# Optimization experiments

Measured on AMD Instinct MI355X. Metric: run time of the kernel, lower is better.

Reference implementation:

```python
import jax, jax.numpy as jnp
import numpy as np

N, T, H, O, S, R = 64, 1024, 256, 80, 128, 2


def _lin(k, fin, fout):
    kw, kb = jax.random.split(k)
    s = 1.0 / np.sqrt(fin)
    return (jax.random.uniform(kw, (fout, fin), jnp.float32, -s, s),
            jax.random.uniform(kb, (fout,), jnp.float32, -s, s))


def _gru_params(k, fin, hid):
    k1, k2, k3, k4 = jax.random.split(k, 4)
    s = 1.0 / np.sqrt(hid)
    u = lambda kk, shp: jax.random.uniform(kk, shp, jnp.float32, -s, s)
    return u(k1, (3 * hid, fin)), u(k2, (3 * hid, hid)), u(k3, (3 * hid,)), u(k4, (3 * hid,))


def setup_inputs() -> dict:
    key = jax.random.key(0)
    ks = jax.random.split(key, 16)
    inp = {}
    inp["input_enc"] = jax.random.normal(ks[0], (N, T, 2 * H), jnp.float32)
    inp["input_attW_enc"] = jax.random.normal(ks[1], (N, T, 2 * H), jnp.float32)
    inp["input_dec"] = jax.random.normal(ks[2], (N, O), jnp.float32)
    inp["style_vec"] = jax.random.normal(ks[3], (N, 1, S), jnp.float32)
    lengths = jnp.sort(jax.random.randint(ks[4], (N,), 1, T + 1))[::-1]
    inp["lengths_enc"] = lengths.at[0].set(T)  # pack_padded requires max(len)==T, descending
    inp["pw1"], inp["pb1"] = _lin(ks[5], O, 2 * H)
    inp["pw2"], inp["pb2"] = _lin(ks[6], 2 * H, H)
    inp["wdec"], inp["bdec"] = _lin(ks[7], 2 * H, 2 * H)
    inp["ga_ih"], inp["ga_hh"], inp["ga_bih"], inp["ga_bhh"] = _gru_params(ks[8], 3 * H + S, 2 * H)
    inp["wattn"], inp["battn"] = _lin(ks[9], 2 * H, 1)
    inp["wsc"], inp["bsc"] = _lin(ks[10], 4 * H + S, 2 * H)
    inp["g1_ih"], inp["g1_hh"], inp["g1_bih"], inp["g1_bhh"] = _gru_params(ks[11], 4 * H + S, 2 * H)
    inp["g2_ih"], inp["g2_hh"], inp["g2_bih"], inp["g2_bhh"] = _gru_params(ks[12], 2 * H, 2 * H)
    inp["wout"], inp["bout"] = _lin(ks[13], 2 * H, R * O)
    return inp


def _gru_cell(x, h, w_ih, w_hh, b_ih, b_hh):
    # PyTorch GRU cell: gates order (r, z, n)
    gi = x @ w_ih.T + b_ih
    gh = h @ w_hh.T + b_hh
    ir, iz, inn = jnp.split(gi, 3, -1)
    hr, hz, hn = jnp.split(gh, 3, -1)
    r = jax.nn.sigmoid(ir + hr)
    z = jax.nn.sigmoid(iz + hz)
    n = jnp.tanh(inn + r * hn)
    return (1.0 - z) * n + z * h


def reference(input_enc, input_attW_enc, input_dec, style_vec,
              pw1, pb1, pw2, pb2, wdec, bdec,
              ga_ih, ga_hh, ga_bih, ga_bhh,
              wattn, battn, wsc, bsc,
              g1_ih, g1_hh, g1_bih, g1_bhh,
              g2_ih, g2_hh, g2_bih, g2_bhh,
              wout, bout, lengths_enc):
    Nn, Tt, D2 = input_enc.shape
    Hh = D2 // 2
    # prenet (dropout disabled: eval-mode reference)
    pre = jax.nn.relu(jax.nn.relu(input_dec @ pw1.T + pb1) @ pw2.T + pb2)  # (N,H)
    ctx0 = jnp.zeros((Nn, 2 * Hh), input_enc.dtype)  # input_context=None -> zeros
    sv = style_vec[:, 0, :]
    x_att = jnp.concatenate([pre, ctx0, sv], axis=-1)  # (N,3H+S)
    h0 = jnp.zeros((Nn, 2 * Hh), input_enc.dtype)  # hidden states start None -> zeros
    out_att = _gru_cell(x_att, h0, ga_ih, ga_hh, ga_bih, ga_bhh)  # (N,2H)
    attW_dec = out_att @ wdec.T + bdec  # (N,2H), broadcast over T (expand_as)
    e = jnp.tanh(input_attW_enc + attW_dec[:, None, :])  # (N,T,2H)
    score = e @ wattn.T + battn  # (N,T,1)
    mask = (jnp.arange(Tt)[None, :] < lengths_enc[:, None]).astype(score.dtype)[..., None]
    w = jnp.exp(score) * mask  # pack/pad zeroes padded positions
    w = w / jnp.maximum(jnp.sum(w, axis=1, keepdims=True), 1e-12)  # F.normalize(p=1, dim=1)
    attn_applied = jnp.einsum('nt,ntd->nd', w[..., 0], input_enc)  # bmm(w^T, enc) -> (N,2H)
    out_dec = jnp.concatenate([attn_applied, out_att, sv], axis=-1)  # (N,4H+S)
    residual = out_dec @ wsc.T + bsc
    h1 = _gru_cell(out_dec, h0, g1_ih, g1_hh, g1_bih, g1_bhh)
    residual = residual + h1
    h2 = _gru_cell(residual, h0, g2_ih, g2_hh, g2_bih, g2_bhh)
    residual = residual + h2
    output = (residual @ wout.T + bout).reshape(Nn, R, -1)  # (N,r,O)
    return output, attn_applied[:, None, :]
```

## Files before the change

### kernel.cpp

```cpp
#include <hip/hip_runtime.h>
#include <math.h>

#define NB  64
#define TT  1024
#define H2  512
#define SS  128
#define OO  80
#define FIN_A 896
#define FIN_1 1152
#define CH  32

__device__ __forceinline__ float fast_rcp(float x) { return __builtin_amdgcn_rcpf(x); }
__device__ __forceinline__ float fast_sigmoid(float x) { return fast_rcp(1.0f + __expf(-x)); }
__device__ __forceinline__ float fast_tanh(float x) {
    float e = __expf(2.0f * x);
    return 1.0f - 2.0f * fast_rcp(e + 1.0f);
}
__device__ __forceinline__ float wred(float p) {
    #pragma unroll
    for (int o = 32; o > 0; o >>= 1) p += __shfl_xor(p, o, 64);
    return p;
}

__global__ void k_l1(const float* __restrict__ xdec, const float* __restrict__ pw1,
                     const float* __restrict__ pb1, const float* __restrict__ sv,
                     float* __restrict__ t1T, float* __restrict__ xaT,
                     float* __restrict__ out_decT) {
    int wv = threadIdx.x >> 6, lane = threadIdx.x & 63;
    if (blockIdx.x < 128) {
        int i = blockIdx.x * 4 + wv;
        const float* w = pw1 + i * OO;
        const float* x = xdec + lane * OO;
        float acc = 0.0f;
        #pragma unroll 8
        for (int k = 0; k < OO; ++k) acc += w[k] * x[k];
        t1T[i * 64 + lane] = fmaxf(acc + pb1[i], 0.0f);
    } else {
        int s = (blockIdx.x - 128) * 4 + wv;
        float v = sv[lane * SS + s];
        xaT[(256 + s) * 64 + lane] = v;
        out_decT[(1024 + s) * 64 + lane] = v;
    }
}

__global__ __launch_bounds__(512) void k_l2(const float* __restrict__ t1T,
                                            const float* __restrict__ pw2,
                                            const float* __restrict__ pb2,
                                            float* __restrict__ xaT) {
    int i = blockIdx.x;
    int wv = threadIdx.x >> 6, lane = threadIdx.x & 63;
    int k0 = wv * 64;
    const float* w = pw2 + (size_t)i * H2 + k0;
    const float* xT = t1T + k0 * 64;
    float p = 0.0f;
    #pragma unroll 8
    for (int k = 0; k < 64; ++k) p += w[k] * xT[k * 64 + lane];
    __shared__ float s[8][64];
    s[wv][lane] = p;
    __syncthreads();
    if (wv == 0) {
        float acc = 0.0f;
        #pragma unroll
        for (int q = 0; q < 8; ++q) acc += s[q][lane];
        xaT[i * 64 + lane] = fmaxf(acc + pb2[i], 0.0f);
    }
}

__global__ __launch_bounds__(512) void k_gruA(const float* __restrict__ xaT,
                                              const float* __restrict__ ga_ih,
                                              const float* __restrict__ ga_bih,
                                              const float* __restrict__ ga_bhh,
                                              float* __restrict__ out_decT) {
    int j = blockIdx.x;
    int wv = threadIdx.x >> 6, lane = threadIdx.x & 63;
    int k0 = wv * 48;
    const float* wr = ga_ih + (size_t)j * FIN_A;
    const float* wz = ga_ih + (size_t)(H2 + j) * FIN_A;
    const float* wn = ga_ih + (size_t)(2 * H2 + j) * FIN_A;
    float pr = 0.0f, pz = 0.0f, pn = 0.0f;
    #pragma unroll 8
    for (int kk = 0; kk < 48; ++kk) {
        int k = k0 + kk;
        int wc = k + (k >= 256 ? 512 : 0);
        float xv = xaT[k * 64 + lane];
        pr += wr[wc] * xv; pz += wz[wc] * xv; pn += wn[wc] * xv;
    }
    __shared__ float s[3][8][64];
    s[0][wv][lane] = pr; s[1][wv][lane] = pz; s[2][wv][lane] = pn;
    __syncthreads();
    if (wv == 0) {
        float fr = 0.0f, fz = 0.0f, fn = 0.0f;
        #pragma unroll
        for (int q = 0; q < 8; ++q) { fr += s[0][q][lane]; fz += s[1][q][lane]; fn += s[2][q][lane]; }
        float r = fast_sigmoid(fr + ga_bih[j] + ga_bhh[j]);
        float z = fast_sigmoid(fz + ga_bih[H2 + j] + ga_bhh[H2 + j]);
        float nn = fast_tanh(fn + ga_bih[2 * H2 + j] + r * ga_bhh[2 * H2 + j]);
        out_decT[(H2 + j) * 64 + lane] = (1.0f - z) * nn;
    }
}

__global__ __launch_bounds__(512) void k_attw(const float* __restrict__ out_decT,
                                              const float* __restrict__ wdec,
                                              const float* __restrict__ bdec,
                                              float* __restrict__ attW_dec) {
    int i = blockIdx.x;
    int wv = threadIdx.x >> 6, lane = threadIdx.x & 63;
    int k0 = wv * 64;
    const float* w = wdec + (size_t)i * H2 + k0;
    const float* xT = out_decT + (H2 + k0) * 64;
    float p = 0.0f;
    #pragma unroll 8
    for (int k = 0; k < 64; ++k) p += w[k] * xT[k * 64 + lane];
    __shared__ float s[8][64];
    s[wv][lane] = p;
    __syncthreads();
    if (wv == 0) {
        float acc = 0.0f;
        #pragma unroll
        for (int q = 0; q < 8; ++q) acc += s[q][lane];
        attW_dec[lane * H2 + i] = acc + bdec[i];
    }
}

__global__ __launch_bounds__(256, 8) void k_attn(
        const float* __restrict__ enc, const float* __restrict__ attw_enc,
        const float* __restrict__ attW_dec, const float* __restrict__ wattn,
        const float* __restrict__ battn, const int* __restrict__ lengths,
        float* __restrict__ num_part ,
        float* __restrict__ den_part ) {
    int n = blockIdx.y, c = blockIdx.x;
    int wv = threadIdx.x >> 6, lane = threadIdx.x & 63;
    int t0 = c * (TT / CH);
    int len = lengths[n];
    __shared__ float sew[TT / CH];
    __shared__ float s[4 * 512];
    __shared__ float sd[4];

    {
        const float4* d4 = (const float4*)(attW_dec + n * H2);
        const float4* w4 = (const float4*)wattn;
        float b = battn[0];
        #pragma unroll
        for (int r = 0; r < 8; ++r) {
            int t = t0 + wv * 8 + r;
            float val = 0.0f;
            if (t < len) {
                const float4* e4 = (const float4*)(attw_enc + ((size_t)(n * TT + t)) * H2);
                float p = 0.0f;
                #pragma unroll
                for (int m = 0; m < 2; ++m) {
                    int idx = lane + m * 64;
                    float4 e = e4[idx], d = d4[idx], w = w4[idx];
                    p += fast_tanh(e.x + d.x) * w.x + fast_tanh(e.y + d.y) * w.y +
                         fast_tanh(e.z + d.z) * w.z + fast_tanh(e.w + d.w) * w.w;
                }
                p = wred(p);
                val = __expf(p + b);
            }
            if (lane == 0) sew[wv * 8 + r] = val;
        }
    }
    __syncthreads();

    int d0 = lane * 8;
    const float* base = enc + ((size_t)(n * TT + t0 + wv * 8)) * H2 + d0;
    float4 a0 = {0, 0, 0, 0}, a1 = {0, 0, 0, 0};
    float dp = 0.0f;
    #pragma unroll
    for (int r = 0; r < 8; ++r) {
        float wt = sew[wv * 8 + r];
        if (wt != 0.0f) {
            const float4* v4 = (const float4*)(base + (size_t)r * H2);
            float4 v0 = v4[0], v1 = v4[1];
            a0.x += wt * v0.x; a0.y += wt * v0.y; a0.z += wt * v0.z; a0.w += wt * v0.w;
            a1.x += wt * v1.x; a1.y += wt * v1.y; a1.z += wt * v1.z; a1.w += wt * v1.w;
            dp += wt;
        }
    }
    float4* srow = (float4*)(s + wv * 512 + d0);
    srow[0] = a0; srow[1] = a1;
    if (lane == 0) sd[wv] = dp;
    __syncthreads();
    int d = threadIdx.x;
    float r0 = s[d] + s[512 + d] + s[1024 + d] + s[1536 + d];
    float r1 = s[256 + d] + s[768 + d] + s[1280 + d] + s[1792 + d];
    num_part[((size_t)c * H2 + d) * 64 + n] = r0;
    num_part[((size_t)c * H2 + 256 + d) * 64 + n] = r1;
    if (threadIdx.x == 0) den_part[c * NB + n] = sd[0] + sd[1] + sd[2] + sd[3];
}

__global__ void k_reduce(const float* __restrict__ num_part, const float* __restrict__ den_part,
                         float* __restrict__ out, float* __restrict__ out_decT) {
    int d = blockIdx.x * 4 + (threadIdx.x >> 6);
    int lane = threadIdx.x & 63;
    float s = 0.0f, den = 0.0f;
    #pragma unroll 8
    for (int c = 0; c < CH; ++c) {
        s += num_part[((size_t)c * H2 + d) * 64 + lane];
        den += den_part[c * NB + lane];
    }
    float a = s / fmaxf(den, 1e-12f);
    out_decT[d * 64 + lane] = a;
    out[NB * 160 + lane * H2 + d] = a;
}

__global__ __launch_bounds__(512) void k_sc_h1(const float* __restrict__ out_decT,
                                               const float* __restrict__ wsc,
                                               const float* __restrict__ bsc,
                                               const float* __restrict__ g1_ih,
                                               const float* __restrict__ g1_bih,
                                               const float* __restrict__ g1_bhh,
                                               float* __restrict__ res1T) {
    int j = blockIdx.x;
    int wv = threadIdx.x >> 6, lane = threadIdx.x & 63;
    int k0 = wv * 144;
    const float* ws_ = wsc + (size_t)j * FIN_1 + k0;
    const float* wr = g1_ih + (size_t)j * FIN_1 + k0;
    const float* wz = g1_ih + (size_t)(H2 + j) * FIN_1 + k0;
    const float* wn = g1_ih + (size_t)(2 * H2 + j) * FIN_1 + k0;
    const float* xT = out_decT + k0 * 64;
    float2 ps = {0, 0}, pr = {0, 0}, pz = {0, 0}, pn = {0, 0};
    #pragma unroll 4
    for (int k = 0; k < 144; k += 2) {
        float x0 = xT[k * 64 + lane];
        float x1 = xT[(k + 1) * 64 + lane];
        float2 a = *(const float2*)(ws_ + k);
        float2 b = *(const float2*)(wr + k);
        float2 cc = *(const float2*)(wz + k);
        float2 dd = *(const float2*)(wn + k);
        ps.x += a.x * x0; ps.y += a.y * x1;
        pr.x += b.x * x0; pr.y += b.y * x1;
        pz.x += cc.x * x0; pz.y += cc.y * x1;
        pn.x += dd.x * x0; pn.y += dd.y * x1;
    }
    __shared__ float s[4][8][64];
    s[0][wv][lane] = ps.x + ps.y; s[1][wv][lane] = pr.x + pr.y;
    s[2][wv][lane] = pz.x + pz.y; s[3][wv][lane] = pn.x + pn.y;
    __syncthreads();
    if (wv == 0) {
        float fs = 0.0f, fr = 0.0f, fz = 0.0f, fn = 0.0f;
        #pragma unroll
        for (int q = 0; q < 8; ++q) {
            fs += s[0][q][lane]; fr += s[1][q][lane];
            fz += s[2][q][lane]; fn += s[3][q][lane];
        }
        float r = fast_sigmoid(fr + g1_bih[j] + g1_bhh[j]);
        float z = fast_sigmoid(fz + g1_bih[H2 + j] + g1_bhh[H2 + j]);
        float nn = fast_tanh(fn + g1_bih[2 * H2 + j] + r * g1_bhh[2 * H2 + j]);
        res1T[j * 64 + lane] = fs + bsc[j] + (1.0f - z) * nn;
    }
}

__global__ __launch_bounds__(512) void k_h2(const float* __restrict__ res1T,
                                            const float* __restrict__ g2_ih,
                                            const float* __restrict__ g2_bih,
                                            const float* __restrict__ g2_bhh,
                                            float* __restrict__ res2T) {
    int j = blockIdx.x;
    int wv = threadIdx.x >> 6, lane = threadIdx.x & 63;
    int k0 = wv * 64;
    const float* wr = g2_ih + (size_t)j * H2 + k0;
    const float* wz = g2_ih + (size_t)(H2 + j) * H2 + k0;
    const float* wn = g2_ih + (size_t)(2 * H2 + j) * H2 + k0;
    const float* xT = res1T + k0 * 64;
    float pr = 0.0f, pz = 0.0f, pn = 0.0f;
    #pragma unroll 8
    for (int k = 0; k < 64; ++k) {
        float xv = xT[k * 64 + lane];
        pr += wr[k] * xv; pz += wz[k] * xv; pn += wn[k] * xv;
    }
    __shared__ float s[3][8][64];
    s[0][wv][lane] = pr; s[1][wv][lane] = pz; s[2][wv][lane] = pn;
    __syncthreads();
    if (wv == 0) {
        float fr = 0.0f, fz = 0.0f, fn = 0.0f;
        #pragma unroll
        for (int q = 0; q < 8; ++q) { fr += s[0][q][lane]; fz += s[1][q][lane]; fn += s[2][q][lane]; }
        float r = fast_sigmoid(fr + g2_bih[j] + g2_bhh[j]);
        float z = fast_sigmoid(fz + g2_bih[H2 + j] + g2_bhh[H2 + j]);
        float nn = fast_tanh(fn + g2_bih[2 * H2 + j] + r * g2_bhh[2 * H2 + j]);
        res2T[j * 64 + lane] = res1T[j * 64 + lane] + (1.0f - z) * nn;
    }
}

__global__ __launch_bounds__(512) void k_out(const float* __restrict__ res2T,
                                             const float* __restrict__ wout,
                                             const float* __restrict__ bout,
                                             float* __restrict__ out) {
    int i = blockIdx.x;
    int wv = threadIdx.x >> 6, lane = threadIdx.x & 63;
    int k0 = wv * 64;
    const float* w = wout + (size_t)i * H2 + k0;
    const float* xT = res2T + k0 * 64;
    float p = 0.0f;
    #pragma unroll 8
    for (int k = 0; k < 64; ++k) p += w[k] * xT[k * 64 + lane];
    __shared__ float s[8][64];
    s[wv][lane] = p;
    __syncthreads();
    if (wv == 0) {
        float acc = 0.0f;
        #pragma unroll
        for (int q = 0; q < 8; ++q) acc += s[q][lane];
        out[lane * 160 + i] = acc + bout[i];
    }
}

extern "C" void kernel_launch(void* const* d_in, const int* in_sizes, int n_in,
                              void* d_out, int out_size, void* d_ws, size_t ws_size,
                              hipStream_t stream) {
    const float* input_enc      = (const float*)d_in[0];
    const float* input_attW_enc = (const float*)d_in[1];
    const float* input_dec      = (const float*)d_in[2];
    const float* style_vec      = (const float*)d_in[3];
    const int*   lengths_enc    = (const int*)d_in[4];
    const float* pw1  = (const float*)d_in[5];
    const float* pb1  = (const float*)d_in[6];
    const float* pw2  = (const float*)d_in[7];
    const float* pb2  = (const float*)d_in[8];
    const float* wdec = (const float*)d_in[9];
    const float* bdec = (const float*)d_in[10];
    const float* ga_ih  = (const float*)d_in[11];
    const float* ga_bih = (const float*)d_in[13];
    const float* ga_bhh = (const float*)d_in[14];
    const float* wattn  = (const float*)d_in[15];
    const float* battn  = (const float*)d_in[16];
    const float* wsc    = (const float*)d_in[17];
    const float* bsc    = (const float*)d_in[18];
    const float* g1_ih  = (const float*)d_in[19];
    const float* g1_bih = (const float*)d_in[21];
    const float* g1_bhh = (const float*)d_in[22];
    const float* g2_ih  = (const float*)d_in[23];
    const float* g2_bih = (const float*)d_in[25];
    const float* g2_bhh = (const float*)d_in[26];
    const float* wout   = (const float*)d_in[27];
    const float* bout   = (const float*)d_in[28];
    float* out = (float*)d_out;

    float* ws = (float*)d_ws;
    float* num_part = ws;
    float* den_part = ws + 1048576;
    float* t1T      = ws + 1050624;
    float* xaT      = ws + 1083392;
    float* out_decT = ws + 1107968;
    float* attW_dec = ws + 1181696;
    float* res1T    = ws + 1214464;
    float* res2T    = ws + 1247232;

    k_l1<<<160, 256, 0, stream>>>(input_dec, pw1, pb1, style_vec, t1T, xaT, out_decT);
    k_l2<<<256, 512, 0, stream>>>(t1T, pw2, pb2, xaT);
    k_gruA<<<512, 512, 0, stream>>>(xaT, ga_ih, ga_bih, ga_bhh, out_decT);
    k_attw<<<512, 512, 0, stream>>>(out_decT, wdec, bdec, attW_dec);
    k_attn<<<dim3(CH, NB), 256, 0, stream>>>(input_enc, input_attW_enc, attW_dec,
                                             wattn, battn, lengths_enc, num_part, den_part);
    k_reduce<<<128, 256, 0, stream>>>(num_part, den_part, out, out_decT);
    k_sc_h1<<<512, 512, 0, stream>>>(out_decT, wsc, bsc, g1_ih, g1_bih, g1_bhh, res1T);
    k_h2<<<512, 512, 0, stream>>>(res1T, g2_ih, g2_bih, g2_bhh, res2T);
    k_out<<<160, 512, 0, stream>>>(res2T, wout, bout, out);
}
```

Before: 388.4 us.

## Pair long and short sequences per attention block and make partial sums row-major

Each attention block now handles two batch rows, n and 63-n, so that long and short sequences (lengths are sorted descending) are paired and per-block work is balanced. The grid is halved to match. The num_part layout changes from transposed to [chunk][n][d], giving coalesced row writes in k_attn and coalesced reads in k_reduce, whose grid is reorganised by (n, d-half). The trade-offs are fewer blocks, which means less parallelism and latency hiding, an extra sync per block, and a strided transposed write to out_decT in k_reduce.

```diff
diff --git a/kernel.cpp b/kernel.cpp
--- a/kernel.cpp
+++ b/kernel.cpp
@@ -122,86 +122,94 @@
     }
 }
 
-__global__ __launch_bounds__(256, 8) void k_attn(
+__global__ __launch_bounds__(256) void k_attn(
         const float* __restrict__ enc, const float* __restrict__ attw_enc,
         const float* __restrict__ attW_dec, const float* __restrict__ wattn,
         const float* __restrict__ battn, const int* __restrict__ lengths,
         float* __restrict__ num_part ,
         float* __restrict__ den_part ) {
-    int n = blockIdx.y, c = blockIdx.x;
+    int p = blockIdx.y;
+    int c = blockIdx.x;
     int wv = threadIdx.x >> 6, lane = threadIdx.x & 63;
     int t0 = c * (TT / CH);
-    int len = lengths[n];
     __shared__ float sew[TT / CH];
     __shared__ float s[4 * 512];
     __shared__ float sd[4];
-
-    {
-        const float4* d4 = (const float4*)(attW_dec + n * H2);
-        const float4* w4 = (const float4*)wattn;
-        float b = battn[0];
+    const float4* w4 = (const float4*)wattn;
+    float b = battn[0];
+
+    #pragma unroll
+    for (int half = 0; half < 2; ++half) {
+        int n = half ? (63 - p) : p;
+        int len = lengths[n];
+
+        {
+            const float4* d4 = (const float4*)(attW_dec + n * H2);
+            #pragma unroll
+            for (int r = 0; r < 8; ++r) {
+                int t = t0 + wv * 8 + r;
+                float val = 0.0f;
+                if (t < len) {
+                    const float4* e4 = (const float4*)(attw_enc + ((size_t)(n * TT + t)) * H2);
+                    float pp = 0.0f;
+                    #pragma unroll
+                    for (int m = 0; m < 2; ++m) {
+                        int idx = lane + m * 64;
+                        float4 e = e4[idx], d = d4[idx], w = w4[idx];
+                        pp += fast_tanh(e.x + d.x) * w.x + fast_tanh(e.y + d.y) * w.y +
+                              fast_tanh(e.z + d.z) * w.z + fast_tanh(e.w + d.w) * w.w;
+                    }
+                    pp = wred(pp);
+                    val = __expf(pp + b);
+                }
+                if (lane == 0) sew[wv * 8 + r] = val;
+            }
+        }
+        __syncthreads();
+
+        int d0 = lane * 8;
+        const float* base = enc + ((size_t)(n * TT + t0 + wv * 8)) * H2 + d0;
+        float4 a0 = {0, 0, 0, 0}, a1 = {0, 0, 0, 0};
+        float dp = 0.0f;
         #pragma unroll
         for (int r = 0; r < 8; ++r) {
-            int t = t0 + wv * 8 + r;
-            float val = 0.0f;
-            if (t < len) {
-                const float4* e4 = (const float4*)(attw_enc + ((size_t)(n * TT + t)) * H2);
-                float p = 0.0f;
-                #pragma unroll
-                for (int m = 0; m < 2; ++m) {
-                    int idx = lane + m * 64;
-                    float4 e = e4[idx], d = d4[idx], w = w4[idx];
-                    p += fast_tanh(e.x + d.x) * w.x + fast_tanh(e.y + d.y) * w.y +
-                         fast_tanh(e.z + d.z) * w.z + fast_tanh(e.w + d.w) * w.w;
-                }
-                p = wred(p);
-                val = __expf(p + b);
+            float wt = sew[wv * 8 + r];
+            if (wt != 0.0f) {
+                const float4* v4 = (const float4*)(base + (size_t)r * H2);
+                float4 v0 = v4[0], v1 = v4[1];
+                a0.x += wt * v0.x; a0.y += wt * v0.y; a0.z += wt * v0.z; a0.w += wt * v0.w;
+                a1.x += wt * v1.x; a1.y += wt * v1.y; a1.z += wt * v1.z; a1.w += wt * v1.w;
+                dp += wt;
             }
-            if (lane == 0) sew[wv * 8 + r] = val;
         }
-    }
-    __syncthreads();
-
-    int d0 = lane * 8;
-    const float* base = enc + ((size_t)(n * TT + t0 + wv * 8)) * H2 + d0;
-    float4 a0 = {0, 0, 0, 0}, a1 = {0, 0, 0, 0};
-    float dp = 0.0f;
-    #pragma unroll
-    for (int r = 0; r < 8; ++r) {
-        float wt = sew[wv * 8 + r];
-        if (wt != 0.0f) {
-            const float4* v4 = (const float4*)(base + (size_t)r * H2);
-            float4 v0 = v4[0], v1 = v4[1];
-            a0.x += wt * v0.x; a0.y += wt * v0.y; a0.z += wt * v0.z; a0.w += wt * v0.w;
-            a1.x += wt * v1.x; a1.y += wt * v1.y; a1.z += wt * v1.z; a1.w += wt * v1.w;
-            dp += wt;
-        }
-    }
-    float4* srow = (float4*)(s + wv * 512 + d0);
-    srow[0] = a0; srow[1] = a1;
-    if (lane == 0) sd[wv] = dp;
-    __syncthreads();
-    int d = threadIdx.x;
-    float r0 = s[d] + s[512 + d] + s[1024 + d] + s[1536 + d];
-    float r1 = s[256 + d] + s[768 + d] + s[1280 + d] + s[1792 + d];
-    num_part[((size_t)c * H2 + d) * 64 + n] = r0;
-    num_part[((size_t)c * H2 + 256 + d) * 64 + n] = r1;
-    if (threadIdx.x == 0) den_part[c * NB + n] = sd[0] + sd[1] + sd[2] + sd[3];
+        float4* srow = (float4*)(s + wv * 512 + d0);
+        srow[0] = a0; srow[1] = a1;
+        if (lane == 0) sd[wv] = dp;
+        __syncthreads();
+        int d = threadIdx.x;
+        float r0 = s[d] + s[512 + d] + s[1024 + d] + s[1536 + d];
+        float r1 = s[256 + d] + s[768 + d] + s[1280 + d] + s[1792 + d];
+        float* np = num_part + ((size_t)(c * NB + n)) * H2;
+        np[d] = r0;
+        np[256 + d] = r1;
+        if (threadIdx.x == 0) den_part[c * NB + n] = sd[0] + sd[1] + sd[2] + sd[3];
+        __syncthreads();
+    }
 }
 
 __global__ void k_reduce(const float* __restrict__ num_part, const float* __restrict__ den_part,
                          float* __restrict__ out, float* __restrict__ out_decT) {
-    int d = blockIdx.x * 4 + (threadIdx.x >> 6);
-    int lane = threadIdx.x & 63;
+    int n = blockIdx.x;
+    int d = blockIdx.y * 256 + threadIdx.x;
     float s = 0.0f, den = 0.0f;
     #pragma unroll 8
     for (int c = 0; c < CH; ++c) {
-        s += num_part[((size_t)c * H2 + d) * 64 + lane];
-        den += den_part[c * NB + lane];
+        s += num_part[((size_t)(c * NB + n)) * H2 + d];
+        den += den_part[c * NB + n];
     }
     float a = s / fmaxf(den, 1e-12f);
-    out_decT[d * 64 + lane] = a;
-    out[NB * 160 + lane * H2 + d] = a;
+    out[NB * 160 + n * H2 + d] = a;
+    out_decT[(size_t)d * 64 + n] = a;
 }
 
 __global__ __launch_bounds__(512) void k_sc_h1(const float* __restrict__ out_decT,
@@ -225,11 +233,11 @@
         float x0 = xT[k * 64 + lane];
         float x1 = xT[(k + 1) * 64 + lane];
         float2 a = *(const float2*)(ws_ + k);
-        float2 b = *(const float2*)(wr + k);
+        float2 bb = *(const float2*)(wr + k);
         float2 cc = *(const float2*)(wz + k);
         float2 dd = *(const float2*)(wn + k);
         ps.x += a.x * x0; ps.y += a.y * x1;
-        pr.x += b.x * x0; pr.y += b.y * x1;
+        pr.x += bb.x * x0; pr.y += bb.y * x1;
         pz.x += cc.x * x0; pz.y += cc.y * x1;
         pn.x += dd.x * x0; pn.y += dd.y * x1;
     }
@@ -351,9 +359,9 @@
     k_l2<<<256, 512, 0, stream>>>(t1T, pw2, pb2, xaT);
     k_gruA<<<512, 512, 0, stream>>>(xaT, ga_ih, ga_bih, ga_bhh, out_decT);
     k_attw<<<512, 512, 0, stream>>>(out_decT, wdec, bdec, attW_dec);
-    k_attn<<<dim3(CH, NB), 256, 0, stream>>>(input_enc, input_attW_enc, attW_dec,
+    k_attn<<<dim3(CH, 32), 256, 0, stream>>>(input_enc, input_attW_enc, attW_dec,
                                              wattn, battn, lengths_enc, num_part, den_part);
-    k_reduce<<<128, 256, 0, stream>>>(num_part, den_part, out, out_decT);
+    k_reduce<<<dim3(64, 2), 256, 0, stream>>>(num_part, den_part, out, out_decT);
     k_sc_h1<<<512, 512, 0, stream>>>(out_decT, wsc, bsc, g1_ih, g1_bih, g1_bhh, res1T);
     k_h2<<<512, 512, 0, stream>>>(res1T, g2_ih, g2_bih, g2_bhh, res2T);
     k_out<<<160, 512, 0, stream>>>(res2T, wout, bout, out);
```

Measured after the change: 383.3 us. No clear change (-1.3%).
